# Kernel tuning notes

Hardware: AMD Instinct MI355X
Metric: run time of the kernel (lower is better)

Reference implementation:

```python
import jax, jax.numpy as jnp
import numpy as np

PAD = 0  # padding_idx for all int feature columns


def setup_inputs() -> dict:
    key = jax.random.key(0)
    ks = jax.random.split(key, 8)
    B = 16384
    return {
        "item_hist": jax.random.randint(ks[0], (B, 50), 0, 100000, dtype=jnp.int64 if jax.config.jax_enable_x64 else jnp.int32).astype(jnp.int32),
        "cate_hist": jax.random.randint(ks[1], (B, 50), 0, 100000).astype(jnp.int32),
        "ctx_ids": jax.random.randint(ks[2], (B, 20), 0, 1000).astype(jnp.int32),
        "price": jax.random.normal(ks[3], (B, 1), dtype=jnp.float32),
        "dense_vec": jax.random.normal(ks[4], (B, 128), dtype=jnp.float32),
        "W_item": jax.random.normal(ks[5], (100000, 64), dtype=jnp.float32),
        "W_cate": jax.random.normal(ks[6], (100000, 64), dtype=jnp.float32),
        "W_ctx": jax.random.normal(ks[7], (1000, 32), dtype=jnp.float32),
    }


def reference(item_hist, cate_hist, ctx_ids, price, dense_vec, W_item, W_cate, W_ctx):
    # torch Embedding with padding_idx: row PAD is zero (and receives no grad)
    Wi = W_item.at[PAD].set(0.0)
    Wc = W_cate.at[PAD].set(0.0)
    Wx = W_ctx.at[PAD].set(0.0)
    # sum merger: [B, L, D] -> [B, D]
    e_item = jnp.take(Wi, item_hist, axis=0).sum(axis=-2)
    # mean merger (divides by L including padding slots, as torch .mean does)
    e_cate = jnp.take(Wc, cate_hist, axis=0).mean(axis=-2)
    # concat merger: [B, L, D] -> [B, L*D]
    B = ctx_ids.shape[0]
    e_ctx = jnp.take(Wx, ctx_ids, axis=0).reshape(B, -1)
    # FeatureLayer concatenates columns in declared order
    return jnp.concatenate([e_item, e_cate, e_ctx, price, dense_vec], axis=-1)
```

## Files before the change

### kernel.cpp

```cpp
#include <hip/hip_runtime.h>


#define LH 50
#define LC 20
#define DI 64
#define DC 64
#define DX 32
#define DDENSE 128
#define OUT_D 897
#define NIT 13
#define ROWS 4
#define BLK_OUT (ROWS * OUT_D)

typedef float f32x4 __attribute__((ext_vector_type(4)));

__global__ __launch_bounds__(256) void featlayer_kernel(
    const int* __restrict__ item_hist,
    const int* __restrict__ cate_hist,
    const int* __restrict__ ctx_ids,
    const float* __restrict__ price,
    const float* __restrict__ dense_vec,
    const float* __restrict__ W_item,
    const float* __restrict__ W_cate,
    const float* __restrict__ W_ctx,
    float* __restrict__ out,
    int B)
{
    __shared__ __align__(16) float obuf[BLK_OUT];
    __shared__ int ih_s[ROWS * LH];
    __shared__ int ch_s[ROWS * LH];
    __shared__ int cx_s[ROWS * LC];

    const int t     = threadIdx.x;
    const int rbase = blockIdx.x * ROWS;

    if (t < ROWS * LH) {
        ih_s[t] = item_hist[(size_t)rbase * LH + t];
        ch_s[t] = cate_hist[(size_t)rbase * LH + t];
    }
    if (t < ROWS * LC) cx_s[t] = ctx_ids[(size_t)rbase * LC + t];

    if (t < 128) {
        const int r = t >> 5;
        const int c = t & 31;
        const f32x4 dvv = *reinterpret_cast<const f32x4*>(
            dense_vec + ((size_t)(rbase + r) * DDENSE + c * 4));
        float* o = obuf + r * OUT_D + (DI + DC + LC * DX + 1) + c * 4;
        o[0] = dvv.x; o[1] = dvv.y; o[2] = dvv.z; o[3] = dvv.w;
    }
    if (t < ROWS) obuf[t * OUT_D + DI + DC + LC * DX] = price[rbase + t];

    __syncthreads();

    const int w    = t >> 6;
    const int lane = t & 63;
    const int sub  = lane >> 4;
    const int l16  = lane & 15;

    int idxI[NIT], idxC[NIT];
    #pragma unroll
    for (int k = 0; k < NIT; ++k) {
        const int ki = sub + 4 * k;
        idxI[k] = (ki < LH) ? ih_s[w * LH + ki] : 0;
        idxC[k] = (ki < LH) ? ch_s[w * LH + ki] : 0;
    }

    f32x4 iacc = {0.f, 0.f, 0.f, 0.f};
    f32x4 cacc = {0.f, 0.f, 0.f, 0.f};
    #pragma unroll
    for (int k = 0; k < NIT; ++k) {
        const f32x4 vi = *reinterpret_cast<const f32x4*>(
            W_item + ((size_t)idxI[k] * DI + l16 * 4));
        const f32x4 vc = *reinterpret_cast<const f32x4*>(
            W_cate + ((size_t)idxC[k] * DC + l16 * 4));
        const float si = (idxI[k] != 0) ? 1.0f : 0.0f;
        const float sc = (idxC[k] != 0) ? 1.0f : 0.0f;
        iacc += vi * si;
        cacc += vc * sc;
    }

    #pragma unroll
    for (int e = 0; e < 4; ++e) {
        float a = iacc[e];
        a += __shfl_xor(a, 16, 64);
        a += __shfl_xor(a, 32, 64);
        iacc[e] = a;
        float c = cacc[e];
        c += __shfl_xor(c, 16, 64);
        c += __shfl_xor(c, 32, 64);
        cacc[e] = c;
    }

    if (sub == 0) {
        float* oi = obuf + w * OUT_D + l16 * 4;
        float* oc = obuf + w * OUT_D + DI + l16 * 4;
        const float inv = 1.0f / (float)LH;
        #pragma unroll
        for (int e = 0; e < 4; ++e) {
            oi[e] = iacc[e];
            oc[e] = cacc[e] * inv;
        }
    }

    #pragma unroll
    for (int t2 = 0; t2 < 3; ++t2) {
        const int c = lane + 64 * t2;
        if (c < (LC * DX) / 4) {
            const int id = cx_s[w * LC + (c >> 3)];
            f32x4 v = {0.f, 0.f, 0.f, 0.f};
            if (id != 0)
                v = *reinterpret_cast<const f32x4*>(
                    W_ctx + ((size_t)id * DX + (c & 7) * 4));
            float* o = obuf + w * OUT_D + DI + DC + 4 * c;
            o[0] = v.x; o[1] = v.y; o[2] = v.z; o[3] = v.w;
        }
    }

    __syncthreads();

    float* __restrict__ oblk = out + (size_t)rbase * OUT_D;
    #pragma unroll
    for (int i = 0; i < 4; ++i) {
        const int c = t + 256 * i;
        if (c < BLK_OUT / 4) {
            const f32x4 v = *reinterpret_cast<const f32x4*>(obuf + 4 * c);
            *reinterpret_cast<f32x4*>(oblk + 4 * c) = v;
        }
    }
}

extern "C" void kernel_launch(void* const* d_in, const int* in_sizes, int n_in,
                              void* d_out, int out_size, void* d_ws, size_t ws_size,
                              hipStream_t stream) {
    const int*   item_hist = (const int*)  d_in[0];
    const int*   cate_hist = (const int*)  d_in[1];
    const int*   ctx_ids   = (const int*)  d_in[2];
    const float* price     = (const float*)d_in[3];
    const float* dense_vec = (const float*)d_in[4];
    const float* W_item    = (const float*)d_in[5];
    const float* W_cate    = (const float*)d_in[6];
    const float* W_ctx     = (const float*)d_in[7];
    float* out = (float*)d_out;

    const int B = in_sizes[0] / LH;
    const int grid = (B + ROWS - 1) / ROWS;
    featlayer_kernel<<<grid, 256, 0, stream>>>(
        item_hist, cate_hist, ctx_ids, price, dense_vec,
        W_item, W_cate, W_ctx, out, B);
}
```

Before: 71.70 us.

## Convert embedding tables to fp16 in workspace and gather half-precision rows

```diff
diff --git a/kernel.cpp b/kernel.cpp
--- a/kernel.cpp
+++ b/kernel.cpp
@@ -8,12 +8,34 @@
 #define DX 32
 #define DDENSE 128
 #define OUT_D 897
-#define NIT 13
 #define ROWS 4
 #define BLK_OUT (ROWS * OUT_D)
-
-typedef float f32x4 __attribute__((ext_vector_type(4)));
-
+#define NROW_TAB 100000
+#define TAB_ELEMS (NROW_TAB * 64)
+#define NIT8 7
+
+typedef float    f32x4 __attribute__((ext_vector_type(4)));
+typedef _Float16 f16x4 __attribute__((ext_vector_type(4)));
+typedef _Float16 f16x8 __attribute__((ext_vector_type(8)));
+
+__global__ __launch_bounds__(256) void convert_tables_kernel(
+    const float* __restrict__ Wi, const float* __restrict__ Wc,
+    _Float16* __restrict__ Hi, _Float16* __restrict__ Hc)
+{
+    const int stride = gridDim.x * blockDim.x;
+    for (int i = blockIdx.x * blockDim.x + threadIdx.x;
+         i < TAB_ELEMS / 4; i += stride) {
+        const f32x4 a = reinterpret_cast<const f32x4*>(Wi)[i];
+        const f32x4 b = reinterpret_cast<const f32x4*>(Wc)[i];
+        f16x4 ha, hb;
+        #pragma unroll
+        for (int e = 0; e < 4; ++e) { ha[e] = (_Float16)a[e]; hb[e] = (_Float16)b[e]; }
+        reinterpret_cast<f16x4*>(Hi)[i] = ha;
+        reinterpret_cast<f16x4*>(Hc)[i] = hb;
+    }
+}
+
+template <bool HALF>
 __global__ __launch_bounds__(256) void featlayer_kernel(
     const int* __restrict__ item_hist,
     const int* __restrict__ cate_hist,
@@ -22,6 +44,8 @@
     const float* __restrict__ dense_vec,
     const float* __restrict__ W_item,
     const float* __restrict__ W_cate,
+    const _Float16* __restrict__ H_item,
+    const _Float16* __restrict__ H_cate,
     const float* __restrict__ W_ctx,
     float* __restrict__ out,
     int B)
@@ -54,51 +78,95 @@
 
     const int w    = t >> 6;
     const int lane = t & 63;
-    const int sub  = lane >> 4;
-    const int l16  = lane & 15;
-
-    int idxI[NIT], idxC[NIT];
-    #pragma unroll
-    for (int k = 0; k < NIT; ++k) {
-        const int ki = sub + 4 * k;
-        idxI[k] = (ki < LH) ? ih_s[w * LH + ki] : 0;
-        idxC[k] = (ki < LH) ? ch_s[w * LH + ki] : 0;
-    }
-
-    f32x4 iacc = {0.f, 0.f, 0.f, 0.f};
-    f32x4 cacc = {0.f, 0.f, 0.f, 0.f};
-    #pragma unroll
-    for (int k = 0; k < NIT; ++k) {
-        const f32x4 vi = *reinterpret_cast<const f32x4*>(
-            W_item + ((size_t)idxI[k] * DI + l16 * 4));
-        const f32x4 vc = *reinterpret_cast<const f32x4*>(
-            W_cate + ((size_t)idxC[k] * DC + l16 * 4));
-        const float si = (idxI[k] != 0) ? 1.0f : 0.0f;
-        const float sc = (idxC[k] != 0) ? 1.0f : 0.0f;
-        iacc += vi * si;
-        cacc += vc * sc;
-    }
-
-    #pragma unroll
-    for (int e = 0; e < 4; ++e) {
-        float a = iacc[e];
-        a += __shfl_xor(a, 16, 64);
-        a += __shfl_xor(a, 32, 64);
-        iacc[e] = a;
-        float c = cacc[e];
-        c += __shfl_xor(c, 16, 64);
-        c += __shfl_xor(c, 32, 64);
-        cacc[e] = c;
-    }
-
-    if (sub == 0) {
-        float* oi = obuf + w * OUT_D + l16 * 4;
-        float* oc = obuf + w * OUT_D + DI + l16 * 4;
-        const float inv = 1.0f / (float)LH;
+
+    if (HALF) {
+        const int sub8 = lane >> 3;
+        const int l8   = lane & 7;
+
+        int idxI[NIT8], idxC[NIT8];
+        #pragma unroll
+        for (int k = 0; k < NIT8; ++k) {
+            const int ki = sub8 + 8 * k;
+            idxI[k] = (ki < LH) ? ih_s[w * LH + ki] : 0;
+            idxC[k] = (ki < LH) ? ch_s[w * LH + ki] : 0;
+        }
+
+        float iacc[8] = {0,0,0,0,0,0,0,0};
+        float cacc[8] = {0,0,0,0,0,0,0,0};
+        #pragma unroll
+        for (int k = 0; k < NIT8; ++k) {
+            const f16x8 vi = *reinterpret_cast<const f16x8*>(
+                H_item + ((size_t)idxI[k] * 64 + l8 * 8));
+            const f16x8 vc = *reinterpret_cast<const f16x8*>(
+                H_cate + ((size_t)idxC[k] * 64 + l8 * 8));
+            const float si = (idxI[k] != 0) ? 1.0f : 0.0f;
+            const float sc = (idxC[k] != 0) ? 1.0f : 0.0f;
+            #pragma unroll
+            for (int e = 0; e < 8; ++e) {
+                iacc[e] += (float)vi[e] * si;
+                cacc[e] += (float)vc[e] * sc;
+            }
+        }
+
+        #pragma unroll
+        for (int e = 0; e < 8; ++e) {
+            float a = iacc[e];
+            a += __shfl_xor(a, 8, 64);
+            a += __shfl_xor(a, 16, 64);
+            a += __shfl_xor(a, 32, 64);
+            iacc[e] = a;
+            float c = cacc[e];
+            c += __shfl_xor(c, 8, 64);
+            c += __shfl_xor(c, 16, 64);
+            c += __shfl_xor(c, 32, 64);
+            cacc[e] = c;
+        }
+
+        if (sub8 == 0) {
+            float* oi = obuf + w * OUT_D + l8 * 8;
+            float* oc = obuf + w * OUT_D + DI + l8 * 8;
+            const float inv = 1.0f / (float)LH;
+            #pragma unroll
+            for (int e = 0; e < 8; ++e) {
+                oi[e] = iacc[e];
+                oc[e] = cacc[e] * inv;
+            }
+        }
+    } else {
+        const int sub = lane >> 4;
+        const int l16 = lane & 15;
+        int idxI[13], idxC[13];
+        #pragma unroll
+        for (int k = 0; k < 13; ++k) {
+            const int ki = sub + 4 * k;
+            idxI[k] = (ki < LH) ? ih_s[w * LH + ki] : 0;
+            idxC[k] = (ki < LH) ? ch_s[w * LH + ki] : 0;
+        }
+        f32x4 iacc = {0,0,0,0}, cacc = {0,0,0,0};
+        #pragma unroll
+        for (int k = 0; k < 13; ++k) {
+            const f32x4 vi = *reinterpret_cast<const f32x4*>(
+                W_item + ((size_t)idxI[k] * DI + l16 * 4));
+            const f32x4 vc = *reinterpret_cast<const f32x4*>(
+                W_cate + ((size_t)idxC[k] * DC + l16 * 4));
+            iacc += vi * ((idxI[k] != 0) ? 1.0f : 0.0f);
+            cacc += vc * ((idxC[k] != 0) ? 1.0f : 0.0f);
+        }
         #pragma unroll
         for (int e = 0; e < 4; ++e) {
-            oi[e] = iacc[e];
-            oc[e] = cacc[e] * inv;
+            float a = iacc[e];
+            a += __shfl_xor(a, 16, 64); a += __shfl_xor(a, 32, 64);
+            iacc[e] = a;
+            float c = cacc[e];
+            c += __shfl_xor(c, 16, 64); c += __shfl_xor(c, 32, 64);
+            cacc[e] = c;
+        }
+        if (sub == 0) {
+            float* oi = obuf + w * OUT_D + l16 * 4;
+            float* oc = obuf + w * OUT_D + DI + l16 * 4;
+            const float inv = 1.0f / (float)LH;
+            #pragma unroll
+            for (int e = 0; e < 4; ++e) { oi[e] = iacc[e]; oc[e] = cacc[e] * inv; }
         }
     }
 
@@ -144,7 +212,18 @@
 
     const int B = in_sizes[0] / LH;
     const int grid = (B + ROWS - 1) / ROWS;
-    featlayer_kernel<<<grid, 256, 0, stream>>>(
-        item_hist, cate_hist, ctx_ids, price, dense_vec,
-        W_item, W_cate, W_ctx, out, B);
+
+    const size_t tab_bytes = (size_t)TAB_ELEMS * sizeof(_Float16);
+    if (ws_size >= 2 * tab_bytes) {
+        _Float16* Hi = (_Float16*)d_ws;
+        _Float16* Hc = Hi + TAB_ELEMS;
+        convert_tables_kernel<<<2048, 256, 0, stream>>>(W_item, W_cate, Hi, Hc);
+        featlayer_kernel<true><<<grid, 256, 0, stream>>>(
+            item_hist, cate_hist, ctx_ids, price, dense_vec,
+            W_item, W_cate, Hi, Hc, W_ctx, out, B);
+    } else {
+        featlayer_kernel<false><<<grid, 256, 0, stream>>>(
+            item_hist, cate_hist, ctx_ids, price, dense_vec,
+            W_item, W_cate, nullptr, nullptr, W_ctx, out, B);
+    }
 }
```

Result: faster. 58.36 us (-18.6%).
